# Performance work log

Hardware: AMD Instinct MI355X
Metric: run time of the kernel (lower is better)

Reference implementation:

```python
import jax, jax.numpy as jnp
import numpy as np
from math import sqrt

MEM_SIZE = 1024
MEM_DIM = 256


def setup_inputs() -> dict:
    key = jax.random.key(0)
    k1, k2, k3 = jax.random.split(key, 3)
    x = jax.random.normal(k1, (8, 256, 64, 64), dtype=jnp.float32)
    mask = jax.random.randint(k2, (8, 1, 64, 64), 0, 2).astype(jnp.bool_)
    mem = jax.random.normal(k3, (1, MEM_DIM, MEM_SIZE), dtype=jnp.float32)
    return {"x": x, "mask": mask, "mem": mem}


def reference(x, mask, mem):
    # masked-detach blend: x.detach() * ~mask + x * mask
    x = jnp.where(mask, x, jax.lax.stop_gradient(x))
    B, K, H, W = x.shape
    xf = x.reshape(B, K, H * W)            # (B, K, N)
    m = mem[0]                              # (K, M) with M = mem_size
    # logits = m_key @ x / sqrt(K)  -> (B, M, N)
    logits = jnp.einsum('km,bkn->bmn', m, xf) / sqrt(K)
    attn = jax.nn.softmax(logits, axis=1)   # softmax over memory axis
    # out = m @ attn -> (B, K, N)
    out = jnp.einsum('km,bmn->bkn', m, attn).reshape(B, K, H, W)
    return (out, logits)
```

## Files before the change

kernel.cpp:

```cpp
#include <hip/hip_runtime.h>
#include <stdint.h>


typedef __attribute__((ext_vector_type(8))) __bf16 bf16x8;
typedef __attribute__((ext_vector_type(4))) float f32x4;

#define BQ 8
#define KD 256
#define MD 1024
#define ND 4096
#define NT 32

__device__ __forceinline__ unsigned short bf16_rne(float f) {
    union { float f; uint32_t u; } c; c.f = f;
    uint32_t u = c.u;
    uint32_t r = (u + 0x7FFFu + ((u >> 16) & 1u)) >> 16;
    return (unsigned short)r;
}

__global__ void prep_mem(const float* __restrict__ mem,
                         unsigned short* __restrict__ mT,
                         unsigned short* __restrict__ mR) {
    const int k = blockIdx.x;
    const int t = threadIdx.x;
    float4 v = reinterpret_cast<const float4*>(mem + (size_t)k * MD)[t];
    unsigned short h0 = bf16_rne(v.x), h1 = bf16_rne(v.y),
                   h2 = bf16_rne(v.z), h3 = bf16_rne(v.w);
    reinterpret_cast<uint2*>(mR + (size_t)k * MD)[t] =
        make_uint2((uint32_t)h0 | ((uint32_t)h1 << 16),
                   (uint32_t)h2 | ((uint32_t)h3 << 16));
    const int mm = t * 4;
    mT[(size_t)(mm + 0) * KD + k] = h0;
    mT[(size_t)(mm + 1) * KD + k] = h1;
    mT[(size_t)(mm + 2) * KD + k] = h2;
    mT[(size_t)(mm + 3) * KD + k] = h3;
}

__global__ __launch_bounds__(512, 4) void fused_attn_mem(
    const float* __restrict__ x,
    const unsigned short* __restrict__ mT,
    const unsigned short* __restrict__ mR,
    float* __restrict__ out,
    float* __restrict__ logits)
{
    __shared__ __align__(16) char lds[65536];
    float* red_max = (float*)(lds + 32768);
    float* red_sum = (float*)(lds + 33792);

    const int tid = threadIdx.x;
    const int w   = tid >> 6;
    const int l   = tid & 63;
    const int l15 = l & 15;
    const int l4  = l >> 4;

    const int bid = blockIdx.x;
    const int b   = bid >> 7;
    const int n0  = (bid & 127) * NT;

    {
        const float* xb = x + (size_t)b * KD * ND + n0;
        const int k  = tid >> 1;
        const int nh = (tid & 1) * 16;
        const float4* src = reinterpret_cast<const float4*>(xb + (size_t)k * ND + nh);
        float4 v0 = src[0], v1 = src[1], v2 = src[2], v3 = src[3];
        float vals[16] = {v0.x, v0.y, v0.z, v0.w, v1.x, v1.y, v1.z, v1.w,
                          v2.x, v2.y, v2.z, v2.w, v3.x, v3.y, v3.z, v3.w};
        #pragma unroll
        for (int j = 0; j < 16; ++j) {
            const int n = nh + j;
            const int off = n * 512 + (((k >> 3) ^ (n & 7)) << 4) + (k & 7) * 2;
            *(unsigned short*)(lds + off) = bf16_rne(vals[j]);
        }
    }
    __syncthreads();

    f32x4 acc[8][2];
    #pragma unroll
    for (int rt = 0; rt < 8; ++rt)
        #pragma unroll
        for (int ct = 0; ct < 2; ++ct)
            acc[rt][ct] = (f32x4){0.f, 0.f, 0.f, 0.f};

    #pragma unroll
    for (int ks = 0; ks < 8; ++ks) {
        const int kk = ks * 32 + l4 * 8;
        bf16x8 bfr[2];
        #pragma unroll
        for (int ct = 0; ct < 2; ++ct) {
            const int n = ct * 16 + l15;
            const int off = n * 512 + (((kk >> 3) ^ (n & 7)) << 4);
            bfr[ct] = *(const bf16x8*)(lds + off);
        }
        #pragma unroll
        for (int rt = 0; rt < 8; ++rt) {
            const int row = w * 128 + rt * 16 + l15;
            const bf16x8 afr = *(const bf16x8*)(mT + (size_t)row * KD + kk);
            acc[rt][0] = __builtin_amdgcn_mfma_f32_16x16x32_bf16(afr, bfr[0], acc[rt][0], 0, 0, 0);
            acc[rt][1] = __builtin_amdgcn_mfma_f32_16x16x32_bf16(afr, bfr[1], acc[rt][1], 0, 0, 0);
        }
    }

    float lmax[2] = {-3e38f, -3e38f};
    #pragma unroll
    for (int rt = 0; rt < 8; ++rt) {
        #pragma unroll
        for (int ct = 0; ct < 2; ++ct) {
            f32x4 v = acc[rt][ct] * 0.0625f;
            acc[rt][ct] = v;
            lmax[ct] = fmaxf(lmax[ct], fmaxf(fmaxf(v[0], v[1]), fmaxf(v[2], v[3])));
        }
    }

    {
        char* sw = lds + 34816 + w * 2048;
        float* lg = logits + (size_t)b * MD * ND + n0;
        #pragma unroll
        for (int rt = 0; rt < 8; ++rt) {
            #pragma unroll
            for (int ct = 0; ct < 2; ++ct) {
                const int n = ct * 16 + l15;
                #pragma unroll
                for (int r = 0; r < 4; ++r) {
                    const int mloc = l4 * 4 + r;
                    const int off = mloc * 128 + (((n >> 2) ^ (mloc & 7)) << 4) + ((n & 3) << 2);
                    *(float*)(sw + off) = acc[rt][ct][r];
                }
            }
            __asm__ volatile("s_waitcnt lgkmcnt(0)" ::: "memory");
            __builtin_amdgcn_sched_barrier(0);
            #pragma unroll
            for (int half = 0; half < 2; ++half) {
                const int mloc = (l >> 3) + half * 8;
                const int q = l & 7;
                const f32x4 v = *(const f32x4*)(sw + mloc * 128 + ((q ^ (mloc & 7)) << 4));
                *(f32x4*)(lg + (size_t)(w * 128 + rt * 16 + mloc) * ND + q * 4) = v;
            }
            __asm__ volatile("s_waitcnt lgkmcnt(0)" ::: "memory");
            __builtin_amdgcn_sched_barrier(0);
        }
    }

    #pragma unroll
    for (int ct = 0; ct < 2; ++ct) {
        float m = lmax[ct];
        m = fmaxf(m, __shfl_xor(m, 16, 64));
        m = fmaxf(m, __shfl_xor(m, 32, 64));
        lmax[ct] = m;
    }
    if (l < 16) {
        red_max[(w * 2 + 0) * 16 + l] = lmax[0];
        red_max[(w * 2 + 1) * 16 + l] = lmax[1];
    }
    __syncthreads();

    float cmax[2];
    #pragma unroll
    for (int ct = 0; ct < 2; ++ct) {
        float m = -3e38f;
        #pragma unroll
        for (int ww = 0; ww < 8; ++ww)
            m = fmaxf(m, red_max[(ww * 2 + ct) * 16 + l15]);
        cmax[ct] = m;
    }

    float lsum[2] = {0.f, 0.f};
    #pragma unroll
    for (int rt = 0; rt < 8; ++rt) {
        #pragma unroll
        for (int ct = 0; ct < 2; ++ct) {
            f32x4 v = acc[rt][ct];
            v[0] = __expf(v[0] - cmax[ct]);
            v[1] = __expf(v[1] - cmax[ct]);
            v[2] = __expf(v[2] - cmax[ct]);
            v[3] = __expf(v[3] - cmax[ct]);
            lsum[ct] += (v[0] + v[1]) + (v[2] + v[3]);
            acc[rt][ct] = v;
        }
    }
    #pragma unroll
    for (int ct = 0; ct < 2; ++ct) {
        float s = lsum[ct];
        s += __shfl_xor(s, 16, 64);
        s += __shfl_xor(s, 32, 64);
        lsum[ct] = s;
    }
    if (l < 16) {
        red_sum[(w * 2 + 0) * 16 + l] = lsum[0];
        red_sum[(w * 2 + 1) * 16 + l] = lsum[1];
    }
    __syncthreads();

    float rs[2];
    #pragma unroll
    for (int ct = 0; ct < 2; ++ct) {
        float s = 0.f;
        #pragma unroll
        for (int ww = 0; ww < 8; ++ww)
            s += red_sum[(ww * 2 + ct) * 16 + l15];
        rs[ct] = 1.0f / s;
    }
    __syncthreads();

    #pragma unroll
    for (int rt = 0; rt < 8; ++rt) {
        #pragma unroll
        for (int ct = 0; ct < 2; ++ct) {
            f32x4 v = acc[rt][ct];
            unsigned short h0 = bf16_rne(v[0] * rs[ct]);
            unsigned short h1 = bf16_rne(v[1] * rs[ct]);
            unsigned short h2 = bf16_rne(v[2] * rs[ct]);
            unsigned short h3 = bf16_rne(v[3] * rs[ct]);
            const int m0 = w * 128 + rt * 16 + l4 * 4;
            const int n  = ct * 16 + l15;
            const int off = n * 2048 + (((m0 >> 3) ^ (n & 7)) << 4) + (m0 & 7) * 2;
            *(uint2*)(lds + off) = make_uint2((uint32_t)h0 | ((uint32_t)h1 << 16),
                                              (uint32_t)h2 | ((uint32_t)h3 << 16));
        }
    }
    __syncthreads();

    f32x4 acc2[2][2];
    #pragma unroll
    for (int rtile = 0; rtile < 2; ++rtile)
        #pragma unroll
        for (int ct = 0; ct < 2; ++ct)
            acc2[rtile][ct] = (f32x4){0.f, 0.f, 0.f, 0.f};

    #pragma unroll 4
    for (int ks = 0; ks < 32; ++ks) {
        const int mk = ks * 32 + l4 * 8;
        bf16x8 b2[2];
        #pragma unroll
        for (int ct = 0; ct < 2; ++ct) {
            const int n = ct * 16 + l15;
            const int off = n * 2048 + (((mk >> 3) ^ (n & 7)) << 4);
            b2[ct] = *(const bf16x8*)(lds + off);
        }
        #pragma unroll
        for (int rtile = 0; rtile < 2; ++rtile) {
            const bf16x8 a2 = *(const bf16x8*)(mR + (size_t)(w * 32 + rtile * 16 + l15) * MD + mk);
            acc2[rtile][0] = __builtin_amdgcn_mfma_f32_16x16x32_bf16(a2, b2[0], acc2[rtile][0], 0, 0, 0);
            acc2[rtile][1] = __builtin_amdgcn_mfma_f32_16x16x32_bf16(a2, b2[1], acc2[rtile][1], 0, 0, 0);
        }
    }

    float* ob = out + (size_t)b * KD * ND + n0;
    #pragma unroll
    for (int rtile = 0; rtile < 2; ++rtile) {
        #pragma unroll
        for (int ct = 0; ct < 2; ++ct) {
            const int n  = ct * 16 + l15;
            const int r0 = w * 32 + rtile * 16 + l4 * 4;
            ob[(size_t)(r0 + 0) * ND + n] = acc2[rtile][ct][0];
            ob[(size_t)(r0 + 1) * ND + n] = acc2[rtile][ct][1];
            ob[(size_t)(r0 + 2) * ND + n] = acc2[rtile][ct][2];
            ob[(size_t)(r0 + 3) * ND + n] = acc2[rtile][ct][3];
        }
    }
}

extern "C" void kernel_launch(void* const* d_in, const int* in_sizes, int n_in,
                              void* d_out, int out_size, void* d_ws, size_t ws_size,
                              hipStream_t stream) {
    (void)in_sizes; (void)n_in; (void)out_size; (void)ws_size;
    const float* x   = (const float*)d_in[0];
    const float* mem = (const float*)d_in[2];

    float* out    = (float*)d_out;
    float* logits = (float*)d_out + (size_t)BQ * KD * ND;

    unsigned short* mT = (unsigned short*)d_ws;
    unsigned short* mR = mT + (size_t)MD * KD;

    prep_mem<<<dim3(256), dim3(256), 0, stream>>>(mem, mT, mR);
    fused_attn_mem<<<dim3(BQ * (ND / NT)), dim3(512), 0, stream>>>(x, mT, mR, out, logits);
}
```

Before: 138.7 us.

## Restage LDS layout, swizzle block order, nontemporal IO and staged output stores

Moves LDS to dynamic allocation (80KB) with separate regions for the x tile and the attention tile, and remaps block indices so consecutive blocks are spread across strips with batch grouped per XCD. Global x loads and logits/out stores become nontemporal, and the output write now goes through a swizzled LDS transpose so each store is a coalesced 128-bit write. __syncthreads are replaced with raw s_barrier plus lgkmcnt waits. The intent is to cut uncoalesced out stores and cache pollution, at the cost of more LDS per block, which may lower occupancy.

Result: slower. 146.6 us (+5.7%).

```diff
diff --git a/kernel.cpp b/kernel.cpp
--- a/kernel.cpp
+++ b/kernel.cpp
@@ -10,6 +10,13 @@
 #define MD 1024
 #define ND 4096
 #define NT 32
+
+#define RAW_BAR() do {                                           \
+    __asm__ volatile("s_waitcnt lgkmcnt(0)" ::: "memory");       \
+    __builtin_amdgcn_sched_barrier(0);                           \
+    __builtin_amdgcn_s_barrier();                                \
+    __builtin_amdgcn_sched_barrier(0);                           \
+} while (0)
 
 __device__ __forceinline__ unsigned short bf16_rne(float f) {
     union { float f; uint32_t u; } c; c.f = f;
@@ -43,9 +50,9 @@
     float* __restrict__ out,
     float* __restrict__ logits)
 {
-    __shared__ __align__(16) char lds[65536];
-    float* red_max = (float*)(lds + 32768);
-    float* red_sum = (float*)(lds + 33792);
+    extern __shared__ char lds[];
+    float* red_max = (float*)(lds + 16384);
+    float* red_sum = (float*)(lds + 17408);
 
     const int tid = threadIdx.x;
     const int w   = tid >> 6;
@@ -54,25 +61,31 @@
     const int l4  = l >> 4;
 
     const int bid = blockIdx.x;
-    const int b   = bid >> 7;
-    const int n0  = (bid & 127) * NT;
+    const int g   = bid & 7;
+    const int j   = bid >> 3;
+    const int strip = g * 16 + (j & 15);
+    const int b     = j >> 4;
+    const int n0    = strip * NT;
 
     {
         const float* xb = x + (size_t)b * KD * ND + n0;
         const int k  = tid >> 1;
         const int nh = (tid & 1) * 16;
-        const float4* src = reinterpret_cast<const float4*>(xb + (size_t)k * ND + nh);
-        float4 v0 = src[0], v1 = src[1], v2 = src[2], v3 = src[3];
-        float vals[16] = {v0.x, v0.y, v0.z, v0.w, v1.x, v1.y, v1.z, v1.w,
-                          v2.x, v2.y, v2.z, v2.w, v3.x, v3.y, v3.z, v3.w};
-        #pragma unroll
-        for (int j = 0; j < 16; ++j) {
-            const int n = nh + j;
+        const f32x4* src = reinterpret_cast<const f32x4*>(xb + (size_t)k * ND + nh);
+        f32x4 v0 = __builtin_nontemporal_load(src + 0);
+        f32x4 v1 = __builtin_nontemporal_load(src + 1);
+        f32x4 v2 = __builtin_nontemporal_load(src + 2);
+        f32x4 v3 = __builtin_nontemporal_load(src + 3);
+        float vals[16] = {v0[0], v0[1], v0[2], v0[3], v1[0], v1[1], v1[2], v1[3],
+                          v2[0], v2[1], v2[2], v2[3], v3[0], v3[1], v3[2], v3[3]};
+        #pragma unroll
+        for (int jj = 0; jj < 16; ++jj) {
+            const int n = nh + jj;
             const int off = n * 512 + (((k >> 3) ^ (n & 7)) << 4) + (k & 7) * 2;
-            *(unsigned short*)(lds + off) = bf16_rne(vals[j]);
-        }
-    }
-    __syncthreads();
+            *(unsigned short*)(lds + off) = bf16_rne(vals[jj]);
+        }
+    }
+    RAW_BAR();
 
     f32x4 acc[8][2];
     #pragma unroll
@@ -112,7 +125,7 @@
     }
 
     {
-        char* sw = lds + 34816 + w * 2048;
+        char* sw = lds + 18432 + w * 2048;
         float* lg = logits + (size_t)b * MD * ND + n0;
         #pragma unroll
         for (int rt = 0; rt < 8; ++rt) {
@@ -133,7 +146,8 @@
                 const int mloc = (l >> 3) + half * 8;
                 const int q = l & 7;
                 const f32x4 v = *(const f32x4*)(sw + mloc * 128 + ((q ^ (mloc & 7)) << 4));
-                *(f32x4*)(lg + (size_t)(w * 128 + rt * 16 + mloc) * ND + q * 4) = v;
+                __builtin_nontemporal_store(v,
+                    (f32x4*)(lg + (size_t)(w * 128 + rt * 16 + mloc) * ND + q * 4));
             }
             __asm__ volatile("s_waitcnt lgkmcnt(0)" ::: "memory");
             __builtin_amdgcn_sched_barrier(0);
@@ -147,11 +161,12 @@
         m = fmaxf(m, __shfl_xor(m, 32, 64));
         lmax[ct] = m;
     }
+    RAW_BAR();
     if (l < 16) {
         red_max[(w * 2 + 0) * 16 + l] = lmax[0];
         red_max[(w * 2 + 1) * 16 + l] = lmax[1];
     }
-    __syncthreads();
+    RAW_BAR();
 
     float cmax[2];
     #pragma unroll
@@ -188,7 +203,7 @@
         red_sum[(w * 2 + 0) * 16 + l] = lsum[0];
         red_sum[(w * 2 + 1) * 16 + l] = lsum[1];
     }
-    __syncthreads();
+    RAW_BAR();
 
     float rs[2];
     #pragma unroll
@@ -199,7 +214,7 @@
             s += red_sum[(ww * 2 + ct) * 16 + l15];
         rs[ct] = 1.0f / s;
     }
-    __syncthreads();
+    RAW_BAR();
 
     #pragma unroll
     for (int rt = 0; rt < 8; ++rt) {
@@ -212,12 +227,12 @@
             unsigned short h3 = bf16_rne(v[3] * rs[ct]);
             const int m0 = w * 128 + rt * 16 + l4 * 4;
             const int n  = ct * 16 + l15;
-            const int off = n * 2048 + (((m0 >> 3) ^ (n & 7)) << 4) + (m0 & 7) * 2;
+            const int off = 16384 + n * 2048 + (((m0 >> 3) ^ (n & 7)) << 4) + (m0 & 7) * 2;
             *(uint2*)(lds + off) = make_uint2((uint32_t)h0 | ((uint32_t)h1 << 16),
                                               (uint32_t)h2 | ((uint32_t)h3 << 16));
         }
     }
-    __syncthreads();
+    RAW_BAR();
 
     f32x4 acc2[2][2];
     #pragma unroll
@@ -233,7 +248,7 @@
         #pragma unroll
         for (int ct = 0; ct < 2; ++ct) {
             const int n = ct * 16 + l15;
-            const int off = n * 2048 + (((mk >> 3) ^ (n & 7)) << 4);
+            const int off = 16384 + n * 2048 + (((mk >> 3) ^ (n & 7)) << 4);
             b2[ct] = *(const bf16x8*)(lds + off);
         }
         #pragma unroll
@@ -243,18 +258,35 @@
             acc2[rtile][1] = __builtin_amdgcn_mfma_f32_16x16x32_bf16(a2, b2[1], acc2[rtile][1], 0, 0, 0);
         }
     }
-
-    float* ob = out + (size_t)b * KD * ND + n0;
-    #pragma unroll
-    for (int rtile = 0; rtile < 2; ++rtile) {
-        #pragma unroll
-        for (int ct = 0; ct < 2; ++ct) {
-            const int n  = ct * 16 + l15;
-            const int r0 = w * 32 + rtile * 16 + l4 * 4;
-            ob[(size_t)(r0 + 0) * ND + n] = acc2[rtile][ct][0];
-            ob[(size_t)(r0 + 1) * ND + n] = acc2[rtile][ct][1];
-            ob[(size_t)(r0 + 2) * ND + n] = acc2[rtile][ct][2];
-            ob[(size_t)(r0 + 3) * ND + n] = acc2[rtile][ct][3];
+    RAW_BAR();
+
+    {
+        char* sw = lds + 18432 + w * 2048;
+        float* ob = out + (size_t)b * KD * ND + n0;
+        #pragma unroll
+        for (int rtile = 0; rtile < 2; ++rtile) {
+            #pragma unroll
+            for (int ct = 0; ct < 2; ++ct) {
+                const int n = ct * 16 + l15;
+                #pragma unroll
+                for (int r = 0; r < 4; ++r) {
+                    const int rr = l4 * 4 + r;
+                    const int off = rr * 128 + (((n >> 2) ^ (rr & 7)) << 4) + ((n & 3) << 2);
+                    *(float*)(sw + off) = acc2[rtile][ct][r];
+                }
+            }
+            __asm__ volatile("s_waitcnt lgkmcnt(0)" ::: "memory");
+            __builtin_amdgcn_sched_barrier(0);
+            #pragma unroll
+            for (int half = 0; half < 2; ++half) {
+                const int rr = (l >> 3) + half * 8;
+                const int q = l & 7;
+                const f32x4 v = *(const f32x4*)(sw + rr * 128 + ((q ^ (rr & 7)) << 4));
+                __builtin_nontemporal_store(v,
+                    (f32x4*)(ob + (size_t)(w * 32 + rtile * 16 + rr) * ND + q * 4));
+            }
+            __asm__ volatile("s_waitcnt lgkmcnt(0)" ::: "memory");
+            __builtin_amdgcn_sched_barrier(0);
         }
     }
 }
@@ -272,6 +304,13 @@
     unsigned short* mT = (unsigned short*)d_ws;
     unsigned short* mR = mT + (size_t)MD * KD;
 
+    static int lds_attr_set = 0;
+    if (!lds_attr_set) {
+        (void)hipFuncSetAttribute(reinterpret_cast<const void*>(&fused_attn_mem),
+                                  hipFuncAttributeMaxDynamicSharedMemorySize, 81920);
+        lds_attr_set = 1;
+    }
+
     prep_mem<<<dim3(256), dim3(256), 0, stream>>>(mem, mT, mR);
-    fused_attn_mem<<<dim3(BQ * (ND / NT)), dim3(512), 0, stream>>>(x, mT, mR, out, logits);
+    fused_attn_mem<<<dim3(BQ * (ND / NT)), dim3(512), 81920, stream>>>(x, mT, mR, out, logits);
 }
```
